# Kernel tuning notes

Hardware: AMD Instinct MI355X
Metric: run time of the kernel (lower is better)

Reference implementation:

```python
import jax, jax.numpy as jnp
import numpy as np

N_NODES = 20000
N_EDGES = 320000
F = 128            # dim == output_dim
L = 3              # num_layers
N_AGG, N_SCALER = 5, 3
POST_IN = F * (N_AGG * N_SCALER + 1)   # cat([x, scaled_agg])

# deg histogram passed to PNAConv -> avg log-degree constant (PyG: mean of log(bin+1))
_DEG_HIST = np.ones(33, dtype=np.float64)
AVG_LOG = float((np.log(np.arange(33) + 1.0) * _DEG_HIST).sum() / _DEG_HIST.sum())


def _init_linear(k, shape):
    # shape (..., fan_in, fan_out); Kaiming-uniform-ish scale on fan_in
    bound = 1.0 / np.sqrt(shape[-2])
    return jax.random.uniform(k, shape, jnp.float32, -bound, bound)


def setup_inputs() -> dict:
    key = jax.random.key(0)
    ks = jax.random.split(key, 10)
    return {
        "x": jax.random.normal(ks[0], (N_NODES, F), jnp.float32),
        "edge_index": jax.random.randint(ks[1], (2, N_EDGES), 0, N_NODES, jnp.int64),
        "W_pre": _init_linear(ks[2], (L, 2 * F, F)),      # pre_nn Linear(2F->F) per layer
        "b_pre": jnp.zeros((L, F), jnp.float32),
        "W_post": _init_linear(ks[3], (L, POST_IN, F)),   # post_nn Linear(16F->F)
        "b_post": jnp.zeros((L, F), jnp.float32),
        "W_lin": _init_linear(ks[4], (L, F, F)),          # PNAConv.lin Linear(F->F)
        "b_lin": jnp.zeros((L, F), jnp.float32),
        "W_out": _init_linear(ks[5], (F, 1)),             # output_layer
        "b_out": jnp.zeros((1,), jnp.float32),
    }


def reference(x, edge_index, W_pre, b_pre, W_post, b_post, W_lin, b_lin, W_out, b_out):
    n = x.shape[0]
    src, dst = edge_index[0], edge_index[1]  # x_j = x[src], x_i = x[dst]; aggregate onto dst

    # degree-based scalers (graph-fixed)
    cnt = jax.ops.segment_sum(jnp.ones((src.shape[0],), x.dtype), dst, num_segments=n)
    deg = jnp.clip(cnt, 1.0)[:, None]           # PyG clamps deg to >= 1
    log_deg = jnp.log(deg + 1.0)
    amp = log_deg / AVG_LOG                     # amplification scaler
    att = AVG_LOG / log_deg                     # attenuation scaler
    iso = (cnt == 0)[:, None]                   # isolated nodes -> min/max aggregates are 0

    for l in range(W_pre.shape[0]):
        # message: pre_nn(cat([x_i, x_j]))  -> [E, F]
        h = jnp.concatenate([x[dst], x[src]], axis=-1) @ W_pre[l] + b_pre[l]

        s = jax.ops.segment_sum(h, dst, num_segments=n)
        mean = s / deg
        mean_sq = jax.ops.segment_sum(h * h, dst, num_segments=n) / deg
        std = jnp.sqrt(jax.nn.relu(mean_sq - mean * mean) + 1e-5)
        mn = jnp.where(iso, 0.0, jax.ops.segment_min(h, dst, num_segments=n))
        mx = jnp.where(iso, 0.0, jax.ops.segment_max(h, dst, num_segments=n))

        agg = jnp.concatenate([mean, s, std, mn, mx], axis=-1)          # [N, 5F]
        scaled = jnp.concatenate([agg, agg * amp, agg * att], axis=-1)  # [N, 15F]

        out = jnp.concatenate([x, scaled], axis=-1) @ W_post[l] + b_post[l]
        x = jax.nn.relu(out @ W_lin[l] + b_lin[l])

    return jnp.squeeze(x @ W_out + b_out)  # target_dim == 1 -> [N]
```

## Files before the change

kernel.cpp:

```cpp
#include <hip/hip_runtime.h>
#include <math.h>

#define NN 20000
#define NE 320000
#define F 128
#define NLAYER 3
#define MPAD 20032
#define CATW 768
#define SCAN_NB 79

typedef unsigned int u32;
typedef unsigned short u16;
typedef __attribute__((ext_vector_type(8))) short bf16x8;
typedef __attribute__((ext_vector_type(4))) float f32x4;

__device__ __forceinline__ u16 f2bf(float f) {
    union { float f; u32 u; } x{f};
    u32 r = x.u + 0x7FFFu + ((x.u >> 16) & 1u);
    return (u16)(r >> 16);
}
__device__ __forceinline__ float bflo(u32 u) { return __uint_as_float(u << 16); }
__device__ __forceinline__ float bfhi(u32 u) { return __uint_as_float(u & 0xFFFF0000u); }

__device__ __forceinline__ void gload16(const u16* g, u16* l) {
    __builtin_amdgcn_global_load_lds(
        (const __attribute__((address_space(1))) void*)g,
        (__attribute__((address_space(3))) void*)l, 16, 0, 0);
}


__global__ void hist_kernel(const int* __restrict__ dst, int* __restrict__ cnt, int e) {
    int i = blockIdx.x * blockDim.x + threadIdx.x;
    if (i < e) atomicAdd(&cnt[dst[i]], 1);
}

__global__ void scan_p1(const int* __restrict__ cnt, int* __restrict__ bsum) {
    __shared__ int sh[256];
    int i = blockIdx.x * 256 + threadIdx.x;
    int t = threadIdx.x;
    sh[t] = (i < NN) ? cnt[i] : 0;
    __syncthreads();
#pragma unroll
    for (int d = 128; d > 0; d >>= 1) {
        if (t < d) sh[t] += sh[t + d];
        __syncthreads();
    }
    if (t == 0) bsum[blockIdx.x] = sh[0];
}

__global__ void scan_p2(int* __restrict__ bsum) {
    __shared__ int sh[128];
    int t = threadIdx.x;
    int v = (t < SCAN_NB) ? bsum[t] : 0;
    sh[t] = v;
    __syncthreads();
#pragma unroll
    for (int d = 1; d < 128; d <<= 1) {
        int x = (t >= d) ? sh[t - d] : 0;
        __syncthreads();
        sh[t] += x;
        __syncthreads();
    }
    if (t < SCAN_NB) bsum[t] = sh[t] - v;
}

__global__ void scan_p3(const int* __restrict__ cnt, const int* __restrict__ bsum,
                        int* __restrict__ off, float* __restrict__ amp,
                        float* __restrict__ att, float avg_log) {
    __shared__ int sh[256];
    int i = blockIdx.x * 256 + threadIdx.x;
    int t = threadIdx.x;
    int v = (i < NN) ? cnt[i] : 0;
    sh[t] = v;
    __syncthreads();
#pragma unroll
    for (int d = 1; d < 256; d <<= 1) {
        int x = (t >= d) ? sh[t - d] : 0;
        __syncthreads();
        sh[t] += x;
        __syncthreads();
    }
    if (i < NN) {
        int incl = sh[t] + bsum[blockIdx.x];
        off[i] = incl - v;
        if (i == NN - 1) off[NN] = incl;
        float deg = fmaxf((float)v, 1.0f);
        float ld = logf(deg + 1.0f);
        amp[i] = ld / avg_log;
        att[i] = avg_log / ld;
    }
}

__global__ void scatter_kernel(const int* __restrict__ src, const int* __restrict__ dst,
                               const int* __restrict__ off, int* __restrict__ cur,
                               int* __restrict__ csr, int e) {
    int i = blockIdx.x * blockDim.x + threadIdx.x;
    if (i < e) {
        int d = dst[i];
        int p = atomicAdd(&cur[d], 1);
        csr[off[d] + p] = src[i];
    }
}


#define P0 2560000L
#define P1 (P0 + 3L * 256 * 128)
#define P2 (P1 + 3L * 128 * 128)
#define P3 (P2 + 3L * 2048 * 128)
#define P4 (P3 + 3L * 256)
#define P5 (P4 + 3L * 128)
#define P6 (P5 + 3L * 2 * 128 * 128)
#define P7 (P6 + 2L * NN)

__global__ void prep_all(const float* __restrict__ x, const float* __restrict__ W_pre,
                         const float* __restrict__ W_lin, const float* __restrict__ W_post,
                         const float* __restrict__ b_pre, const float* __restrict__ b_post,
                         const float* __restrict__ b_lin,
                         u16* __restrict__ xbuf, u16* __restrict__ cat,
                         u16* __restrict__ WpreT, u16* __restrict__ WlinT,
                         u16* __restrict__ Wpostb, float* __restrict__ biaspre,
                         float* __restrict__ bcomb, u16* __restrict__ BtK,
                         int* __restrict__ cnt, int* __restrict__ cur) {
    long i = (long)blockIdx.x * 256 + threadIdx.x;
    if (i < P0) {
        u16 h = f2bf(x[i]);
        xbuf[i] = h;
        cat[(size_t)(i >> 7) * CATW + (i & 127)] = h;
    } else if (i < P1) {
        long j = i - P0;
        int l = j / 32768, t = j % 32768;
        int c = t >> 7, k = t & 127;
        int si = (c < 128) ? (k * 128 + c) : ((k + 128) * 128 + (c - 128));
        WpreT[l * 32768 + t] = f2bf(W_pre[l * 32768 + si]);
    } else if (i < P2) {
        long j = i - P1;
        int l = j / 16384, t = j % 16384;
        int c = t >> 7, k = t & 127;
        WlinT[l * 16384 + t] = f2bf(W_lin[l * 16384 + k * 128 + c]);
    } else if (i < P3) {
        long j = i - P2;
        Wpostb[j] = f2bf(W_post[j]);
    } else if (i < P4) {
        long j = i - P3;
        int l = j / 256, t = j % 256;
        biaspre[l * 256 + t] = (t < 128) ? b_pre[l * 128 + t] : 0.f;
    } else if (i < P5) {
        long j = i - P4;
        int l = j / 128, t = j % 128;
        float s = b_lin[l * 128 + t];
        for (int c = 0; c < 128; ++c) s += b_post[l * 128 + c] * W_lin[l * 16384 + c * 128 + t];
        bcomb[l * 128 + t] = s;
    } else if (i < P6) {
        long j = i - P5;
        int l = j / 32768, t = j % 32768;
        int gg = 1 + (t >> 14);
        int row = (t >> 7) & 127, k = t & 127;
        BtK[(size_t)l * 294912 + (size_t)(gg * 128 + row) * 768 + k] = 0;
    } else if (i < P7) {
        long j = i - P6;
        if (j < NN) cnt[j] = 0; else cur[j - NN] = 0;
    }
}


#define PROC(u) { float v_; \
    v_ = bflo(u); s0 += v_; q0 = fmaf(v_, v_, q0); mn0 = fminf(mn0, v_); mx0 = fmaxf(mx0, v_); \
    v_ = bfhi(u); s1 += v_; q1 = fmaf(v_, v_, q1); mn1 = fminf(mn1, v_); mx1 = fmaxf(mx1, v_); }

__global__ __launch_bounds__(256) void agg_kernel(
    const u16* __restrict__ preout, const int* __restrict__ off,
    const int* __restrict__ csr, u16* __restrict__ cat) {
    int node = blockIdx.x;
    int tid = threadIdx.x, w = tid >> 6, lane = tid & 63;
    int o0 = off[node], o1 = off[node + 1];
    const u32* bpl = (const u32*)preout + 64 + lane;
    float s0 = 0, s1 = 0, q0 = 0, q1 = 0;
    float mn0 = 1e30f, mn1 = 1e30f, mx0 = -1e30f, mx1 = -1e30f;
    int j = o0 + w;
    for (; j + 12 < o1; j += 16) {
        int i0 = csr[j], i1 = csr[j + 4], i2 = csr[j + 8], i3 = csr[j + 12];
        u32 u0 = bpl[(size_t)i0 * 128];
        u32 u1 = bpl[(size_t)i1 * 128];
        u32 u2 = bpl[(size_t)i2 * 128];
        u32 u3 = bpl[(size_t)i3 * 128];
        PROC(u0); PROC(u1); PROC(u2); PROC(u3);
    }
    for (; j < o1; j += 4) { u32 u = bpl[(size_t)csr[j] * 128]; PROC(u); }

    __shared__ float red[8][256];
    red[0][tid] = s0; red[1][tid] = s1; red[2][tid] = q0; red[3][tid] = q1;
    red[4][tid] = mn0; red[5][tid] = mn1; red[6][tid] = mx0; red[7][tid] = mx1;
    __syncthreads();
    if (w != 0) return;

    s0 = 0; s1 = 0; q0 = 0; q1 = 0;
    mn0 = 1e30f; mn1 = 1e30f; mx0 = -1e30f; mx1 = -1e30f;
#pragma unroll
    for (int ww = 0; ww < 4; ++ww) {
        int sl = ww * 64 + lane;
        s0 += red[0][sl]; s1 += red[1][sl];
        q0 += red[2][sl]; q1 += red[3][sl];
        mn0 = fminf(mn0, red[4][sl]); mn1 = fminf(mn1, red[5][sl]);
        mx0 = fmaxf(mx0, red[6][sl]); mx1 = fmaxf(mx1, red[7][sl]);
    }

    int degi = o1 - o0;
    float mean0, mean1, sum0, sum1, std0, std1, lo0, lo1, hi0, hi1;
    if (degi == 0) {
        sum0 = sum1 = 0.f; mean0 = mean1 = 0.f;
        std0 = std1 = sqrtf(1e-5f);
        lo0 = lo1 = hi0 = hi1 = 0.f;
    } else {
        u32 uc = ((const u32*)preout)[(size_t)node * 128 + lane];
        float c0 = bflo(uc), c1 = bfhi(uc), dg = (float)degi;
        sum0 = dg * c0 + s0; mean0 = sum0 / dg;
        sum1 = dg * c1 + s1; mean1 = sum1 / dg;
        float msq0 = c0 * c0 + (2.f * c0 * s0 + q0) / dg;
        float msq1 = c1 * c1 + (2.f * c1 * s1 + q1) / dg;
        std0 = sqrtf(fmaxf(msq0 - mean0 * mean0, 0.f) + 1e-5f);
        std1 = sqrtf(fmaxf(msq1 - mean1 * mean1, 0.f) + 1e-5f);
        lo0 = c0 + mn0; lo1 = c1 + mn1; hi0 = c0 + mx0; hi1 = c1 + mx1;
    }
    u32* cr = (u32*)cat + (size_t)node * (CATW / 2) + 64 + lane;
    float f0[5] = {mean0, sum0, std0, lo0, hi0};
    float f1[5] = {mean1, sum1, std1, lo1, hi1};
#pragma unroll
    for (int a = 0; a < 5; ++a)
        cr[a * 64] = (u32)f2bf(f0[a]) | ((u32)f2bf(f1[a]) << 16);
}


template <bool BIAS, int MODE, bool SWZ>
__global__ __launch_bounds__(256) void mfma_gemm(
    const u16* __restrict__ A, int lda,
    const u16* __restrict__ Bt, int K,
    const float* __restrict__ bias,
    u16* __restrict__ C, int ldc, int Mreal,
    size_t aS, size_t bS, size_t cS) {
    __shared__ u16 As[64 * 32];
    __shared__ u16 Bs[128 * 32];
    int row0, col0;
    if (SWZ) {
        int g = blockIdx.x;
        int row = (g >> 4) * 8 + (g & 7);
        if (row >= 313) return;
        row0 = row * 64;
        col0 = ((g >> 3) & 1) * 128;
    } else {
        row0 = blockIdx.x * 64;
        col0 = blockIdx.y * 128;
    }
    int z = blockIdx.z;
    A += (size_t)z * aS; Bt += (size_t)z * bS; C += (size_t)z * cS;
    int tid = threadIdx.x;
    int w = tid >> 6, lane = tid & 63;

    int arow = tid >> 2, asl = tid & 3;
    const u16* agp = A + (size_t)(row0 + arow) * lda + ((asl ^ ((arow >> 1) & 3)) << 3);
    u16* alds = As + w * 512;
    int br0 = tid >> 2;
    int br1 = 64 + (tid >> 2);
    const u16* bgp0 = Bt + (size_t)(col0 + br0) * K + (((tid & 3) ^ ((br0 >> 1) & 3)) << 3);
    const u16* bgp1 = Bt + (size_t)(col0 + br1) * K + (((tid & 3) ^ ((br1 >> 1) & 3)) << 3);
    u16* blds0 = Bs + w * 512;
    u16* blds1 = Bs + 2048 + w * 512;

    f32x4 acc[2][4];
#pragma unroll
    for (int m = 0; m < 2; ++m)
#pragma unroll
        for (int n = 0; n < 4; ++n) acc[m][n] = (f32x4){0.f, 0.f, 0.f, 0.f};

    int s = lane >> 4, r = lane & 15;
    int wr = (w >> 1) * 32, wc = (w & 1) * 64;

    for (int k0 = 0; k0 < K; k0 += 32) {
        gload16(agp + k0, alds);
        gload16(bgp0 + k0, blds0);
        gload16(bgp1 + k0, blds1);
        __syncthreads();
        bf16x8 a[2], b[4];
#pragma unroll
        for (int m = 0; m < 2; ++m) {
            int row = wr + m * 16 + r;
            a[m] = *(const bf16x8*)&As[row * 32 + ((s ^ ((row >> 1) & 3)) << 3)];
        }
#pragma unroll
        for (int n = 0; n < 4; ++n) {
            int col = wc + n * 16 + r;
            b[n] = *(const bf16x8*)&Bs[col * 32 + ((s ^ ((col >> 1) & 3)) << 3)];
        }
#pragma unroll
        for (int m = 0; m < 2; ++m)
#pragma unroll
            for (int n = 0; n < 4; ++n)
                acc[m][n] = __builtin_amdgcn_mfma_f32_16x16x32_bf16(a[m], b[n], acc[m][n], 0, 0, 0);
        __syncthreads();
    }

#pragma unroll
    for (int m = 0; m < 2; ++m) {
#pragma unroll
        for (int n = 0; n < 4; ++n) {
            int gcol = col0 + wc + n * 16 + r;
            float bs = BIAS ? bias[gcol] : 0.f;
#pragma unroll
            for (int j = 0; j < 4; ++j) {
                int grow = row0 + wr + m * 16 + s * 4 + j;
                if (grow < Mreal) {
                    u16 h = f2bf(acc[m][n][j] + bs);
                    if (MODE == 0) {
                        C[(size_t)grow * ldc + gcol] = h;
                    } else {
                        size_t idx;
                        if (gcol < 128) idx = (size_t)grow * 768 + gcol;
                        else {
                            int t2 = gcol - 128;
                            int gg = t2 / 640;
                            int ko = 128 + t2 - gg * 640;
                            idx = (size_t)(gg * 128 + grow) * 768 + ko;
                        }
                        C[idx] = h;
                    }
                }
            }
        }
    }
}


__global__ __launch_bounds__(256) void comb2(
    const u16* __restrict__ A,
    const u16* __restrict__ BtK,
    const float* __restrict__ bias,
    const float* __restrict__ amp, const float* __restrict__ att,
    u16* __restrict__ xout,
    u16* __restrict__ catout) {
    __shared__ u16 S[3][8192];
    int g = blockIdx.x;
    int row = (g >> 4) * 8 + (g & 7);
    if (row >= 313) return;
    int row0 = row * 64;
    int cb = (g >> 3) & 1;
    int tid = threadIdx.x;
    int w = tid >> 6, lane = tid & 63;
    int r = lane & 15, s4 = lane >> 4;
    int wr = (w >> 1) * 32, wc = (w & 1) * 32;

    const u16* gp[4];
#pragma unroll
    for (int p = 0; p < 4; ++p) {
        int lid = tid + 256 * p;
        int rt = lid >> 2, q = lid & 3;
        int koff = (q ^ ((rt >> 1) & 3)) << 3;
        if (rt < 64) gp[p] = A + (size_t)(row0 + rt) * 768 + koff;
        else {
            int rb = rt - 64, gg = rb >> 6, jj = rb & 63;
            gp[p] = BtK + (size_t)(gg * 128 + cb * 64 + jj) * 768 + koff;
        }
    }

    f32x4 acc[2][3][2];
#pragma unroll
    for (int m = 0; m < 2; ++m)
#pragma unroll
        for (int gg = 0; gg < 3; ++gg)
#pragma unroll
            for (int n = 0; n < 2; ++n) acc[m][gg][n] = (f32x4){0.f, 0.f, 0.f, 0.f};

    auto STAGE = [&](int t, int b) {
#pragma unroll
        for (int p = 0; p < 4; ++p)
            gload16(gp[p] + t * 32, &S[b][(size_t)(tid + 256 * p) * 8]);
    };

    STAGE(0, 0);
    STAGE(1, 1);
    asm volatile("s_waitcnt vmcnt(4)" ::: "memory");
    __builtin_amdgcn_s_barrier();
    asm volatile("" ::: "memory");

    int buf = 0;
    for (int t = 0; t < 24; ++t) {
        if (t + 2 < 24) STAGE(t + 2, (t + 2) % 3);
        const u16* Sb = S[buf];
        bf16x8 a[2];
#pragma unroll
        for (int m = 0; m < 2; ++m) {
            int rw = wr + m * 16 + r;
            a[m] = *(const bf16x8*)&Sb[rw * 32 + ((s4 ^ ((rw >> 1) & 3)) << 3)];
        }
#pragma unroll
        for (int gg = 0; gg < 3; ++gg)
#pragma unroll
            for (int n = 0; n < 2; ++n) {
                int rowb = 64 + gg * 64 + wc + n * 16 + r;
                bf16x8 b = *(const bf16x8*)&Sb[rowb * 32 + ((s4 ^ ((rowb >> 1) & 3)) << 3)];
#pragma unroll
                for (int m = 0; m < 2; ++m)
                    acc[m][gg][n] = __builtin_amdgcn_mfma_f32_16x16x32_bf16(a[m], b, acc[m][gg][n], 0, 0, 0);
            }
        if (t < 23) {
            if (t + 2 < 24) asm volatile("s_waitcnt vmcnt(4)" ::: "memory");
            else            asm volatile("s_waitcnt vmcnt(0)" ::: "memory");
            __builtin_amdgcn_s_barrier();
            asm volatile("" ::: "memory");
        }
        buf = (buf == 2) ? 0 : buf + 1;
    }

    int gcb = cb * 64 + wc;
#pragma unroll
    for (int m = 0; m < 2; ++m)
#pragma unroll
        for (int j = 0; j < 4; ++j) {
            int grow = row0 + wr + m * 16 + s4 * 4 + j;
            if (grow < NN) {
                float av = amp[grow], tv = att[grow];
#pragma unroll
                for (int n = 0; n < 2; ++n) {
                    int gcol = gcb + n * 16 + r;
                    float v = acc[m][0][n][j] + av * acc[m][1][n][j] + tv * acc[m][2][n][j] + bias[gcol];
                    v = fmaxf(v, 0.f);
                    u16 h = f2bf(v);
                    xout[(size_t)grow * F + gcol] = h;
                    catout[(size_t)grow * CATW + gcol] = h;
                }
            }
        }
}


__global__ void out_kernel(const u16* __restrict__ x, const float* __restrict__ Wout,
                           const float* __restrict__ bout, float* __restrict__ y) {
    int gid = blockIdx.x * blockDim.x + threadIdx.x;
    int wid = gid >> 6, lane = threadIdx.x & 63;
    if (wid >= NN) return;
    u32 u = *(const u32*)&x[(size_t)wid * F + 2 * lane];
    float v = bflo(u) * Wout[2 * lane] + bfhi(u) * Wout[2 * lane + 1];
#pragma unroll
    for (int o = 32; o > 0; o >>= 1) v += __shfl_down(v, o, 64);
    if (lane == 0) y[wid] = v + bout[0];
}


extern "C" void kernel_launch(void* const* d_in, const int* in_sizes, int n_in,
                              void* d_out, int out_size, void* d_ws, size_t ws_size,
                              hipStream_t stream) {
    const float* x_in   = (const float*)d_in[0];
    const int*   ei     = (const int*)d_in[1];
    const float* W_pre  = (const float*)d_in[2];
    const float* b_pre  = (const float*)d_in[3];
    const float* W_post = (const float*)d_in[4];
    const float* b_post = (const float*)d_in[5];
    const float* W_lin  = (const float*)d_in[6];
    const float* b_lin  = (const float*)d_in[7];
    const float* W_out  = (const float*)d_in[8];
    const float* b_out  = (const float*)d_in[9];

    const int* src = ei;
    const int* dst = ei + NE;

    double sl = 0.0;
    for (int i = 0; i < 33; ++i) sl += log((double)(i + 1));
    float avg_log = (float)(sl / 33.0);

    char* ws = (char*)d_ws;
    size_t p = 0;
    auto alloc = [&](size_t bytes) { void* r = ws + p; p += (bytes + 255) & ~(size_t)255; return r; };
    u16*   cat     = (u16*)alloc((size_t)MPAD * CATW * 2);
    u16*   xbuf    = (u16*)alloc((size_t)MPAD * F * 2);
    u16*   preout  = (u16*)alloc((size_t)MPAD * 256 * 2);
    u16*   WpreT   = (u16*)alloc((size_t)3 * 256 * 128 * 2);
    u16*   Wpostb  = (u16*)alloc((size_t)3 * 2048 * 128 * 2);
    u16*   WlinT   = (u16*)alloc((size_t)3 * 128 * 128 * 2);
    u16*   BtK     = (u16*)alloc((size_t)3 * 384 * 768 * 2);
    float* biaspre = (float*)alloc((size_t)3 * 256 * 4);
    float* bcomb   = (float*)alloc((size_t)3 * 128 * 4);
    float* amp     = (float*)alloc((size_t)MPAD * 4);
    float* att     = (float*)alloc((size_t)MPAD * 4);
    int*   cnt     = (int*)alloc((size_t)NN * 4);
    int*   offs    = (int*)alloc((size_t)(NN + 1) * 4);
    int*   cur     = (int*)alloc((size_t)NN * 4);
    int*   csr     = (int*)alloc((size_t)NE * 4);
    int*   bsum    = (int*)alloc((size_t)SCAN_NB * 4);
    (void)ws_size;

    prep_all<<<(int)((P7 + 255) / 256), 256, 0, stream>>>(
        x_in, W_pre, W_lin, W_post, b_pre, b_post, b_lin,
        xbuf, cat, WpreT, WlinT, Wpostb, biaspre, bcomb, BtK, cnt, cur);

    hist_kernel<<<(NE + 255) / 256, 256, 0, stream>>>(dst, cnt, NE);
    scan_p1<<<SCAN_NB, 256, 0, stream>>>(cnt, bsum);
    scan_p2<<<1, 128, 0, stream>>>(bsum);
    scan_p3<<<SCAN_NB, 256, 0, stream>>>(cnt, bsum, offs, amp, att, avg_log);
    scatter_kernel<<<(NE + 255) / 256, 256, 0, stream>>>(src, dst, offs, cur, csr, NE);

    mfma_gemm<false, 1, false><<<dim3(2, 16, 3), 256, 0, stream>>>(
        WlinT, 128, Wpostb, 128, nullptr, BtK, 0, 128,
        16384, 262144, 294912);

    mfma_gemm<true, 0, true><<<640, 256, 0, stream>>>(
        xbuf, F, WpreT, 128, biaspre, preout, 256, MPAD, 0, 0, 0);

    for (int l = 0; l < NLAYER; ++l) {
        agg_kernel<<<NN, 256, 0, stream>>>(preout, offs, csr, cat);
        comb2<<<640, 256, 0, stream>>>(
            cat, BtK + (size_t)l * 294912, bcomb + (size_t)l * 128,
            amp, att, xbuf, cat);
        if (l < NLAYER - 1) {
            mfma_gemm<true, 0, true><<<640, 256, 0, stream>>>(
                xbuf, F, WpreT + (size_t)(l + 1) * 32768, 128,
                biaspre + (size_t)(l + 1) * 256, preout, 256, MPAD, 0, 0, 0);
        }
    }

    out_kernel<<<5000, 256, 0, stream>>>(xbuf, W_out, b_out, (float*)d_out);
}
```

Measured before the change: 251.3 us.

## Split concat buffer and restructure combine GEMM with register-fed A tiles

Replaces the packed concat buffer with separate x and aggregate buffers, so the x tile no longer has to be copied into the concat layout and the zero padding of the combined weight no longer has to be initialised. The combine kernel now uses 128-row tiles. It loads its A operand straight from global memory into registers with one-step prefetch, and stages only B through a 4-buffer LDS ring. It skips the amp and att MFMAs for the x-only K range. The larger tiles give only 320 blocks, which may leave CUs unevenly loaded, and the in-place xbuf read and write across the two column-half blocks remains a race hazard.

```diff
diff --git a/kernel.cpp b/kernel.cpp
--- a/kernel.cpp
+++ b/kernel.cpp
@@ -6,7 +6,7 @@
 #define F 128
 #define NLAYER 3
 #define MPAD 20032
-#define CATW 768
+#define MROW 20096
 #define SCAN_NB 79
 
 typedef unsigned int u32;
@@ -109,23 +109,20 @@
 #define P3 (P2 + 3L * 2048 * 128)
 #define P4 (P3 + 3L * 256)
 #define P5 (P4 + 3L * 128)
-#define P6 (P5 + 3L * 2 * 128 * 128)
-#define P7 (P6 + 2L * NN)
+#define P6 (P5 + 2L * NN)
 
 __global__ void prep_all(const float* __restrict__ x, const float* __restrict__ W_pre,
                          const float* __restrict__ W_lin, const float* __restrict__ W_post,
                          const float* __restrict__ b_pre, const float* __restrict__ b_post,
                          const float* __restrict__ b_lin,
-                         u16* __restrict__ xbuf, u16* __restrict__ cat,
+                         u16* __restrict__ xbuf,
                          u16* __restrict__ WpreT, u16* __restrict__ WlinT,
                          u16* __restrict__ Wpostb, float* __restrict__ biaspre,
-                         float* __restrict__ bcomb, u16* __restrict__ BtK,
+                         float* __restrict__ bcomb,
                          int* __restrict__ cnt, int* __restrict__ cur) {
     long i = (long)blockIdx.x * 256 + threadIdx.x;
     if (i < P0) {
-        u16 h = f2bf(x[i]);
-        xbuf[i] = h;
-        cat[(size_t)(i >> 7) * CATW + (i & 127)] = h;
+        xbuf[i] = f2bf(x[i]);
     } else if (i < P1) {
         long j = i - P0;
         int l = j / 32768, t = j % 32768;
@@ -152,12 +149,6 @@
         bcomb[l * 128 + t] = s;
     } else if (i < P6) {
         long j = i - P5;
-        int l = j / 32768, t = j % 32768;
-        int gg = 1 + (t >> 14);
-        int row = (t >> 7) & 127, k = t & 127;
-        BtK[(size_t)l * 294912 + (size_t)(gg * 128 + row) * 768 + k] = 0;
-    } else if (i < P7) {
-        long j = i - P6;
         if (j < NN) cnt[j] = 0; else cur[j - NN] = 0;
     }
 }
@@ -169,7 +160,7 @@
 
 __global__ __launch_bounds__(256) void agg_kernel(
     const u16* __restrict__ preout, const int* __restrict__ off,
-    const int* __restrict__ csr, u16* __restrict__ cat) {
+    const int* __restrict__ csr, u16* __restrict__ aggb) {
     int node = blockIdx.x;
     int tid = threadIdx.x, w = tid >> 6, lane = tid & 63;
     int o0 = off[node], o1 = off[node + 1];
@@ -221,7 +212,7 @@
         std1 = sqrtf(fmaxf(msq1 - mean1 * mean1, 0.f) + 1e-5f);
         lo0 = c0 + mn0; lo1 = c1 + mn1; hi0 = c0 + mx0; hi1 = c1 + mx1;
     }
-    u32* cr = (u32*)cat + (size_t)node * (CATW / 2) + 64 + lane;
+    u32* cr = (u32*)aggb + (size_t)node * 320 + lane;
     float f0[5] = {mean0, sum0, std0, lo0, hi0};
     float f1[5] = {mean1, sum1, std1, lo1, hi1};
 #pragma unroll
@@ -329,89 +320,99 @@
 }
 
 
-__global__ __launch_bounds__(256) void comb2(
-    const u16* __restrict__ A,
+__global__ __launch_bounds__(256) void comb4(
+    const u16* __restrict__ xbuf,
+    const u16* __restrict__ aggb,
     const u16* __restrict__ BtK,
     const float* __restrict__ bias,
     const float* __restrict__ amp, const float* __restrict__ att,
-    u16* __restrict__ xout,
-    u16* __restrict__ catout) {
-    __shared__ u16 S[3][8192];
+    u16* __restrict__ xout) {
+    __shared__ u16 S[4][6144];
     int g = blockIdx.x;
     int row = (g >> 4) * 8 + (g & 7);
-    if (row >= 313) return;
-    int row0 = row * 64;
+    if (row >= 157) return;
+    int row0 = row * 128;
     int cb = (g >> 3) & 1;
     int tid = threadIdx.x;
     int w = tid >> 6, lane = tid & 63;
     int r = lane & 15, s4 = lane >> 4;
-    int wr = (w >> 1) * 32, wc = (w & 1) * 32;
-
-    const u16* gp[4];
-#pragma unroll
-    for (int p = 0; p < 4; ++p) {
+    int wr = (w >> 1) * 64, wc = (w & 1) * 32;
+
+    const u16* gpB[3];
+#pragma unroll
+    for (int p = 0; p < 3; ++p) {
         int lid = tid + 256 * p;
         int rt = lid >> 2, q = lid & 3;
+        int gg = rt >> 6, jj = rt & 63;
         int koff = (q ^ ((rt >> 1) & 3)) << 3;
-        if (rt < 64) gp[p] = A + (size_t)(row0 + rt) * 768 + koff;
-        else {
-            int rb = rt - 64, gg = rb >> 6, jj = rb & 63;
-            gp[p] = BtK + (size_t)(gg * 128 + cb * 64 + jj) * 768 + koff;
-        }
-    }
-
-    f32x4 acc[2][3][2];
-#pragma unroll
-    for (int m = 0; m < 2; ++m)
+        gpB[p] = BtK + (size_t)(gg * 128 + cb * 64 + jj) * 768 + koff;
+    }
+
+    const u16* aX[4];
+    const u16* aG[4];
+#pragma unroll
+    for (int m = 0; m < 4; ++m) {
+        int rw = row0 + wr + m * 16 + r;
+        aX[m] = xbuf + (size_t)rw * 128 + s4 * 8;
+        aG[m] = aggb + (size_t)rw * 640 + s4 * 8 - 128;
+    }
+
+    f32x4 acc[4][3][2];
+#pragma unroll
+    for (int m = 0; m < 4; ++m)
 #pragma unroll
         for (int gg = 0; gg < 3; ++gg)
 #pragma unroll
             for (int n = 0; n < 2; ++n) acc[m][gg][n] = (f32x4){0.f, 0.f, 0.f, 0.f};
 
-    auto STAGE = [&](int t, int b) {
-#pragma unroll
-        for (int p = 0; p < 4; ++p)
-            gload16(gp[p] + t * 32, &S[b][(size_t)(tid + 256 * p) * 8]);
-    };
-
-    STAGE(0, 0);
-    STAGE(1, 1);
-    asm volatile("s_waitcnt vmcnt(4)" ::: "memory");
-    __builtin_amdgcn_s_barrier();
-    asm volatile("" ::: "memory");
-
-    int buf = 0;
+    bf16x8 acur[4], anext[4];
+
+#pragma unroll
+    for (int m = 0; m < 4; ++m) acur[m] = *(const bf16x8*)(aX[m]);
+#pragma unroll
+    for (int p = 0; p < 3; ++p) gload16(gpB[p], &S[0][(size_t)(tid + 256 * p) * 8]);
+#pragma unroll
+    for (int p = 0; p < 3; ++p) gload16(gpB[p] + 32, &S[1][(size_t)(tid + 256 * p) * 8]);
+
     for (int t = 0; t < 24; ++t) {
-        if (t + 2 < 24) STAGE(t + 2, (t + 2) % 3);
-        const u16* Sb = S[buf];
-        bf16x8 a[2];
-#pragma unroll
-        for (int m = 0; m < 2; ++m) {
-            int rw = wr + m * 16 + r;
-            a[m] = *(const bf16x8*)&Sb[rw * 32 + ((s4 ^ ((rw >> 1) & 3)) << 3)];
-        }
-#pragma unroll
-        for (int gg = 0; gg < 3; ++gg)
+        if (t + 1 < 24) {
+            int kk = (t + 1) * 32;
+#pragma unroll
+            for (int m = 0; m < 4; ++m)
+                anext[m] = (t + 1 < 4) ? *(const bf16x8*)(aX[m] + kk)
+                                       : *(const bf16x8*)(aG[m] + kk);
+        }
+        if (t + 2 < 24) {
+            int kk = (t + 2) * 32;
+#pragma unroll
+            for (int p = 0; p < 3; ++p)
+                gload16(gpB[p] + kk, &S[(t + 2) & 3][(size_t)(tid + 256 * p) * 8]);
+        }
+        if (t < 23) asm volatile("s_waitcnt vmcnt(10)" ::: "memory");
+        else        asm volatile("s_waitcnt vmcnt(0)" ::: "memory");
+        __builtin_amdgcn_s_barrier();
+        asm volatile("" ::: "memory");
+
+        const u16* Sb = S[t & 3];
+#pragma unroll
+        for (int gg = 0; gg < 3; ++gg) {
+            if (gg > 0 && t < 4) continue;
 #pragma unroll
             for (int n = 0; n < 2; ++n) {
-                int rowb = 64 + gg * 64 + wc + n * 16 + r;
-                bf16x8 b = *(const bf16x8*)&Sb[rowb * 32 + ((s4 ^ ((rowb >> 1) & 3)) << 3)];
-#pragma unroll
-                for (int m = 0; m < 2; ++m)
-                    acc[m][gg][n] = __builtin_amdgcn_mfma_f32_16x16x32_bf16(a[m], b, acc[m][gg][n], 0, 0, 0);
+                int rb = gg * 64 + wc + n * 16 + r;
+                bf16x8 b = *(const bf16x8*)&Sb[rb * 32 + ((s4 ^ ((rb >> 1) & 3)) << 3)];
+#pragma unroll
+                for (int m = 0; m < 4; ++m)
+                    acc[m][gg][n] = __builtin_amdgcn_mfma_f32_16x16x32_bf16(acur[m], b, acc[m][gg][n], 0, 0, 0);
             }
-        if (t < 23) {
-            if (t + 2 < 24) asm volatile("s_waitcnt vmcnt(4)" ::: "memory");
-            else            asm volatile("s_waitcnt vmcnt(0)" ::: "memory");
-            __builtin_amdgcn_s_barrier();
-            asm volatile("" ::: "memory");
-        }
-        buf = (buf == 2) ? 0 : buf + 1;
+        }
+#pragma unroll
+        for (int m = 0; m < 4; ++m) acur[m] = anext[m];
     }
 
     int gcb = cb * 64 + wc;
 #pragma unroll
-    for (int m = 0; m < 2; ++m)
+    for (int m = 0; m < 4; ++m)
 #pragma unroll
         for (int j = 0; j < 4; ++j) {
             int grow = row0 + wr + m * 16 + s4 * 4 + j;
@@ -422,9 +423,7 @@
                     int gcol = gcb + n * 16 + r;
                     float v = acc[m][0][n][j] + av * acc[m][1][n][j] + tv * acc[m][2][n][j] + bias[gcol];
                     v = fmaxf(v, 0.f);
-                    u16 h = f2bf(v);
-                    xout[(size_t)grow * F + gcol] = h;
-                    catout[(size_t)grow * CATW + gcol] = h;
+                    xout[(size_t)grow * F + gcol] = f2bf(v);
                 }
             }
         }
@@ -468,8 +467,8 @@
     char* ws = (char*)d_ws;
     size_t p = 0;
     auto alloc = [&](size_t bytes) { void* r = ws + p; p += (bytes + 255) & ~(size_t)255; return r; };
-    u16*   cat     = (u16*)alloc((size_t)MPAD * CATW * 2);
-    u16*   xbuf    = (u16*)alloc((size_t)MPAD * F * 2);
+    u16*   xbuf    = (u16*)alloc((size_t)MROW * F * 2);
+    u16*   aggb    = (u16*)alloc((size_t)MROW * 640 * 2);
     u16*   preout  = (u16*)alloc((size_t)MPAD * 256 * 2);
     u16*   WpreT   = (u16*)alloc((size_t)3 * 256 * 128 * 2);
     u16*   Wpostb  = (u16*)alloc((size_t)3 * 2048 * 128 * 2);
@@ -486,9 +485,9 @@
     int*   bsum    = (int*)alloc((size_t)SCAN_NB * 4);
     (void)ws_size;
 
-    prep_all<<<(int)((P7 + 255) / 256), 256, 0, stream>>>(
+    prep_all<<<(int)((P6 + 255) / 256), 256, 0, stream>>>(
         x_in, W_pre, W_lin, W_post, b_pre, b_post, b_lin,
-        xbuf, cat, WpreT, WlinT, Wpostb, biaspre, bcomb, BtK, cnt, cur);
+        xbuf, WpreT, WlinT, Wpostb, biaspre, bcomb, cnt, cur);
 
     hist_kernel<<<(NE + 255) / 256, 256, 0, stream>>>(dst, cnt, NE);
     scan_p1<<<SCAN_NB, 256, 0, stream>>>(cnt, bsum);
@@ -504,10 +503,10 @@
         xbuf, F, WpreT, 128, biaspre, preout, 256, MPAD, 0, 0, 0);
 
     for (int l = 0; l < NLAYER; ++l) {
-        agg_kernel<<<NN, 256, 0, stream>>>(preout, offs, csr, cat);
-        comb2<<<640, 256, 0, stream>>>(
-            cat, BtK + (size_t)l * 294912, bcomb + (size_t)l * 128,
-            amp, att, xbuf, cat);
+        agg_kernel<<<NN, 256, 0, stream>>>(preout, offs, csr, aggb);
+        comb4<<<320, 256, 0, stream>>>(
+            xbuf, aggb, BtK + (size_t)l * 294912, bcomb + (size_t)l * 128,
+            amp, att, xbuf);
         if (l < NLAYER - 1) {
             mfma_gemm<true, 0, true><<<640, 256, 0, stream>>>(
                 xbuf, F, WpreT + (size_t)(l + 1) * 32768, 128,
```

New measurement: 282.3 us. 12.3% more time.

## Split concat buffer into separate x and aggregate buffers, skip zero MFMA blocks

Applied to the files above, without the earlier changes.

Replaces the combined 768-wide concat buffer with a separate bf16 x buffer and a 640-wide aggregate buffer. The combine GEMM now stages its A tiles from the x buffer for the first four k-tiles and from the aggregate buffer for the rest. For those first four k-tiles it skips the amp and att MFMA groups, so the zeroed weight regions and the prep pass that cleared them are no longer needed. The duplicate store of x into the concat buffer goes away, and the aggregation kernel gives each wave a contiguous chunk of edges instead of a strided interleave. This may change memory locality and how evenly edges are balanced across waves in the aggregation step.

```diff
diff --git a/kernel.cpp b/kernel.cpp
--- a/kernel.cpp
+++ b/kernel.cpp
@@ -6,7 +6,6 @@
 #define F 128
 #define NLAYER 3
 #define MPAD 20032
-#define CATW 768
 #define SCAN_NB 79
 
 typedef unsigned int u32;
@@ -109,23 +108,20 @@
 #define P3 (P2 + 3L * 2048 * 128)
 #define P4 (P3 + 3L * 256)
 #define P5 (P4 + 3L * 128)
-#define P6 (P5 + 3L * 2 * 128 * 128)
-#define P7 (P6 + 2L * NN)
+#define P6 (P5 + 2L * NN)
 
 __global__ void prep_all(const float* __restrict__ x, const float* __restrict__ W_pre,
                          const float* __restrict__ W_lin, const float* __restrict__ W_post,
                          const float* __restrict__ b_pre, const float* __restrict__ b_post,
                          const float* __restrict__ b_lin,
-                         u16* __restrict__ xbuf, u16* __restrict__ cat,
+                         u16* __restrict__ xbuf,
                          u16* __restrict__ WpreT, u16* __restrict__ WlinT,
                          u16* __restrict__ Wpostb, float* __restrict__ biaspre,
-                         float* __restrict__ bcomb, u16* __restrict__ BtK,
+                         float* __restrict__ bcomb,
                          int* __restrict__ cnt, int* __restrict__ cur) {
     long i = (long)blockIdx.x * 256 + threadIdx.x;
     if (i < P0) {
-        u16 h = f2bf(x[i]);
-        xbuf[i] = h;
-        cat[(size_t)(i >> 7) * CATW + (i & 127)] = h;
+        xbuf[i] = f2bf(x[i]);
     } else if (i < P1) {
         long j = i - P0;
         int l = j / 32768, t = j % 32768;
@@ -152,12 +148,6 @@
         bcomb[l * 128 + t] = s;
     } else if (i < P6) {
         long j = i - P5;
-        int l = j / 32768, t = j % 32768;
-        int gg = 1 + (t >> 14);
-        int row = (t >> 7) & 127, k = t & 127;
-        BtK[(size_t)l * 294912 + (size_t)(gg * 128 + row) * 768 + k] = 0;
-    } else if (i < P7) {
-        long j = i - P6;
         if (j < NN) cnt[j] = 0; else cur[j - NN] = 0;
     }
 }
@@ -169,23 +159,27 @@
 
 __global__ __launch_bounds__(256) void agg_kernel(
     const u16* __restrict__ preout, const int* __restrict__ off,
-    const int* __restrict__ csr, u16* __restrict__ cat) {
+    const int* __restrict__ csr, u16* __restrict__ aggb) {
     int node = blockIdx.x;
     int tid = threadIdx.x, w = tid >> 6, lane = tid & 63;
     int o0 = off[node], o1 = off[node + 1];
+    int deg = o1 - o0;
+    int chunk = (deg + 3) >> 2;
+    int b0 = o0 + w * chunk;
+    int b1 = min(b0 + chunk, o1);
     const u32* bpl = (const u32*)preout + 64 + lane;
     float s0 = 0, s1 = 0, q0 = 0, q1 = 0;
     float mn0 = 1e30f, mn1 = 1e30f, mx0 = -1e30f, mx1 = -1e30f;
-    int j = o0 + w;
-    for (; j + 12 < o1; j += 16) {
-        int i0 = csr[j], i1 = csr[j + 4], i2 = csr[j + 8], i3 = csr[j + 12];
+    int j = b0;
+    for (; j + 4 <= b1; j += 4) {
+        int i0 = csr[j], i1 = csr[j + 1], i2 = csr[j + 2], i3 = csr[j + 3];
         u32 u0 = bpl[(size_t)i0 * 128];
         u32 u1 = bpl[(size_t)i1 * 128];
         u32 u2 = bpl[(size_t)i2 * 128];
         u32 u3 = bpl[(size_t)i3 * 128];
         PROC(u0); PROC(u1); PROC(u2); PROC(u3);
     }
-    for (; j < o1; j += 4) { u32 u = bpl[(size_t)csr[j] * 128]; PROC(u); }
+    for (; j < b1; ++j) { u32 u = bpl[(size_t)csr[j] * 128]; PROC(u); }
 
     __shared__ float red[8][256];
     red[0][tid] = s0; red[1][tid] = s1; red[2][tid] = q0; red[3][tid] = q1;
@@ -204,7 +198,7 @@
         mx0 = fmaxf(mx0, red[6][sl]); mx1 = fmaxf(mx1, red[7][sl]);
     }
 
-    int degi = o1 - o0;
+    int degi = deg;
     float mean0, mean1, sum0, sum1, std0, std1, lo0, lo1, hi0, hi1;
     if (degi == 0) {
         sum0 = sum1 = 0.f; mean0 = mean1 = 0.f;
@@ -221,7 +215,7 @@
         std1 = sqrtf(fmaxf(msq1 - mean1 * mean1, 0.f) + 1e-5f);
         lo0 = c0 + mn0; lo1 = c1 + mn1; hi0 = c0 + mx0; hi1 = c1 + mx1;
     }
-    u32* cr = (u32*)cat + (size_t)node * (CATW / 2) + 64 + lane;
+    u32* cr = (u32*)aggb + (size_t)node * 320 + lane;
     float f0[5] = {mean0, sum0, std0, lo0, hi0};
     float f1[5] = {mean1, sum1, std1, lo1, hi1};
 #pragma unroll
@@ -330,12 +324,12 @@
 
 
 __global__ __launch_bounds__(256) void comb2(
-    const u16* __restrict__ A,
+    const u16* __restrict__ xbuf,
+    const u16* __restrict__ aggb,
     const u16* __restrict__ BtK,
     const float* __restrict__ bias,
     const float* __restrict__ amp, const float* __restrict__ att,
-    u16* __restrict__ xout,
-    u16* __restrict__ catout) {
+    u16* __restrict__ xout) {
     __shared__ u16 S[3][8192];
     int g = blockIdx.x;
     int row = (g >> 4) * 8 + (g & 7);
@@ -347,17 +341,18 @@
     int r = lane & 15, s4 = lane >> 4;
     int wr = (w >> 1) * 32, wc = (w & 1) * 32;
 
-    const u16* gp[4];
-#pragma unroll
-    for (int p = 0; p < 4; ++p) {
+    int rtA = tid >> 2, qA = tid & 3;
+    int koffA = (qA ^ ((rtA >> 1) & 3)) << 3;
+    const u16* xA = xbuf + (size_t)(row0 + rtA) * 128 + koffA;
+    const u16* gA = aggb + (size_t)(row0 + rtA) * 640 + koffA - 128;
+    const u16* bB[3];
+#pragma unroll
+    for (int p = 1; p < 4; ++p) {
         int lid = tid + 256 * p;
         int rt = lid >> 2, q = lid & 3;
+        int rb = rt - 64, gg = rb >> 6, jj = rb & 63;
         int koff = (q ^ ((rt >> 1) & 3)) << 3;
-        if (rt < 64) gp[p] = A + (size_t)(row0 + rt) * 768 + koff;
-        else {
-            int rb = rt - 64, gg = rb >> 6, jj = rb & 63;
-            gp[p] = BtK + (size_t)(gg * 128 + cb * 64 + jj) * 768 + koff;
-        }
+        bB[p - 1] = BtK + (size_t)(gg * 128 + cb * 64 + jj) * 768 + koff;
     }
 
     f32x4 acc[2][3][2];
@@ -369,9 +364,11 @@
             for (int n = 0; n < 2; ++n) acc[m][gg][n] = (f32x4){0.f, 0.f, 0.f, 0.f};
 
     auto STAGE = [&](int t, int b) {
-#pragma unroll
-        for (int p = 0; p < 4; ++p)
-            gload16(gp[p] + t * 32, &S[b][(size_t)(tid + 256 * p) * 8]);
+        const u16* a = (t < 4) ? (xA + t * 32) : (gA + t * 32);
+        gload16(a, &S[b][(size_t)tid * 8]);
+#pragma unroll
+        for (int p = 1; p < 4; ++p)
+            gload16(bB[p - 1] + t * 32, &S[b][(size_t)(tid + 256 * p) * 8]);
     };
 
     STAGE(0, 0);
@@ -391,7 +388,8 @@
             a[m] = *(const bf16x8*)&Sb[rw * 32 + ((s4 ^ ((rw >> 1) & 3)) << 3)];
         }
 #pragma unroll
-        for (int gg = 0; gg < 3; ++gg)
+        for (int gg = 0; gg < 3; ++gg) {
+            if (gg > 0 && t < 4) continue;
 #pragma unroll
             for (int n = 0; n < 2; ++n) {
                 int rowb = 64 + gg * 64 + wc + n * 16 + r;
@@ -400,6 +398,7 @@
                 for (int m = 0; m < 2; ++m)
                     acc[m][gg][n] = __builtin_amdgcn_mfma_f32_16x16x32_bf16(a[m], b, acc[m][gg][n], 0, 0, 0);
             }
+        }
         if (t < 23) {
             if (t + 2 < 24) asm volatile("s_waitcnt vmcnt(4)" ::: "memory");
             else            asm volatile("s_waitcnt vmcnt(0)" ::: "memory");
@@ -422,9 +421,7 @@
                     int gcol = gcb + n * 16 + r;
                     float v = acc[m][0][n][j] + av * acc[m][1][n][j] + tv * acc[m][2][n][j] + bias[gcol];
                     v = fmaxf(v, 0.f);
-                    u16 h = f2bf(v);
-                    xout[(size_t)grow * F + gcol] = h;
-                    catout[(size_t)grow * CATW + gcol] = h;
+                    xout[(size_t)grow * F + gcol] = f2bf(v);
                 }
             }
         }
@@ -468,8 +465,8 @@
     char* ws = (char*)d_ws;
     size_t p = 0;
     auto alloc = [&](size_t bytes) { void* r = ws + p; p += (bytes + 255) & ~(size_t)255; return r; };
-    u16*   cat     = (u16*)alloc((size_t)MPAD * CATW * 2);
     u16*   xbuf    = (u16*)alloc((size_t)MPAD * F * 2);
+    u16*   aggb    = (u16*)alloc((size_t)MPAD * 640 * 2);
     u16*   preout  = (u16*)alloc((size_t)MPAD * 256 * 2);
     u16*   WpreT   = (u16*)alloc((size_t)3 * 256 * 128 * 2);
     u16*   Wpostb  = (u16*)alloc((size_t)3 * 2048 * 128 * 2);
@@ -486,9 +483,9 @@
     int*   bsum    = (int*)alloc((size_t)SCAN_NB * 4);
     (void)ws_size;
 
-    prep_all<<<(int)((P7 + 255) / 256), 256, 0, stream>>>(
+    prep_all<<<(int)((P6 + 255) / 256), 256, 0, stream>>>(
         x_in, W_pre, W_lin, W_post, b_pre, b_post, b_lin,
-        xbuf, cat, WpreT, WlinT, Wpostb, biaspre, bcomb, BtK, cnt, cur);
+        xbuf, WpreT, WlinT, Wpostb, biaspre, bcomb, cnt, cur);
 
     hist_kernel<<<(NE + 255) / 256, 256, 0, stream>>>(dst, cnt, NE);
     scan_p1<<<SCAN_NB, 256, 0, stream>>>(cnt, bsum);
@@ -504,10 +501,10 @@
         xbuf, F, WpreT, 128, biaspre, preout, 256, MPAD, 0, 0, 0);
 
     for (int l = 0; l < NLAYER; ++l) {
-        agg_kernel<<<NN, 256, 0, stream>>>(preout, offs, csr, cat);
+        agg_kernel<<<NN, 256, 0, stream>>>(preout, offs, csr, aggb);
         comb2<<<640, 256, 0, stream>>>(
-            cat, BtK + (size_t)l * 294912, bcomb + (size_t)l * 128,
-            amp, att, xbuf, cat);
+            xbuf, aggb, BtK + (size_t)l * 294912, bcomb + (size_t)l * 128,
+            amp, att, xbuf);
         if (l < NLAYER - 1) {
             mfma_gemm<true, 0, true><<<640, 256, 0, stream>>>(
                 xbuf, F, WpreT + (size_t)(l + 1) * 32768, 128,
```

Result: no change. 247.2 us (-1.6%).
